# Kernel tuning notes

Hardware: AMD Instinct MI355X
Metric: run time of the kernel (lower is better)

Reference implementation:

```python
import jax, jax.numpy as jnp
import numpy as np

N = 100000      # nodes
E = 1600000     # edges (avg degree 16)
IN = 128        # in_channels
C = 32          # out_channels per head
H = 4           # heads
NEG_SLOPE = 0.2 # PyG GATConv leaky_relu slope


def setup_inputs() -> dict:
    key = jax.random.key(0)
    k = jax.random.split(key, 6)
    x = jax.random.normal(k[0], (N, IN), jnp.float32)
    edge_index = jax.random.randint(k[1], (2, E), 0, N, jnp.int32)
    # glorot-ish init for learned params
    W = jax.random.normal(k[2], (IN, H * C), jnp.float32) * (2.0 / (IN + H * C)) ** 0.5
    att_src = jax.random.normal(k[3], (H, C), jnp.float32) * (1.0 / C) ** 0.5
    att_dst = jax.random.normal(k[4], (H, C), jnp.float32) * (1.0 / C) ** 0.5
    bias = jnp.zeros((C,), jnp.float32)
    return {"x": x, "edge_index": edge_index, "W": W,
            "att_src": att_src, "att_dst": att_dst, "bias": bias}


def reference(x, edge_index, W, att_src, att_dst, bias):
    n = x.shape[0]
    h_heads, c = att_src.shape
    # add self loops (PyG GATConv default add_self_loops=True)
    loop = jnp.arange(n, dtype=edge_index.dtype)
    src = jnp.concatenate([edge_index[0], loop])
    dst = jnp.concatenate([edge_index[1], loop])
    # shared linear projection for src and dst (single-tensor input in PyG)
    h = (x @ W).reshape(n, h_heads, c)                 # [N,H,C]
    a_src = jnp.sum(h * att_src, axis=-1)              # [N,H]
    a_dst = jnp.sum(h * att_dst, axis=-1)              # [N,H]
    # per-edge attention logits
    e = jax.nn.leaky_relu(a_src[src] + a_dst[dst], NEG_SLOPE)  # [E',H]
    # segment softmax over incoming edges of each dst node
    m = jax.ops.segment_max(e, dst, num_segments=n)    # [N,H]
    m = jax.lax.stop_gradient(jnp.where(jnp.isfinite(m), m, 0.0))
    p = jnp.exp(e - m[dst])
    denom = jax.ops.segment_sum(p, dst, num_segments=n)
    alpha = p / (denom[dst] + 1e-16)                   # [E',H]
    # weighted message scatter-add
    msg = h[src] * alpha[:, :, None]                   # [E',H,C]
    out = jax.ops.segment_sum(msg, dst, num_segments=n)  # [N,H,C]
    out = out.mean(axis=1) + bias                      # concat=False -> head mean
    return jax.nn.relu(out)                            # trailing act layer
```

## Files before the change

kernel.cpp:

```cpp
#include <hip/hip_runtime.h>

#define NODES 100000
#define NEDGE 1600000
#define ET (NEDGE + NODES)
#define INC 128
#define CC 32
#define HH 4
#define NEG 0.2f
#define NB 98

typedef __attribute__((ext_vector_type(8))) short short8;
typedef __attribute__((ext_vector_type(4))) float f32x4;
typedef __attribute__((ext_vector_type(8))) unsigned short u16x8;

static __device__ inline unsigned short f2bf(float f) {
    unsigned u = __float_as_uint(f);
    u += 0x7FFFu + ((u >> 16) & 1u);
    return (unsigned short)(u >> 16);
}
static __device__ inline float bf2f(unsigned short s) {
    return __uint_as_float((unsigned)s << 16);
}
static __device__ inline float lexp(float v) {
    v = v > 0.f ? v : NEG * v;
    return __expf(v);
}

__global__ __launch_bounds__(256) void k_proj(const float* __restrict__ x,
        const float* __restrict__ W, const float* __restrict__ att_src,
        const float* __restrict__ att_dst, unsigned short* __restrict__ hb,
        float* __restrict__ av) {
    __shared__ unsigned short Wt[128][136];
    __shared__ unsigned short Axt[8][128];
    const int tid = threadIdx.x;

    for (int i = tid; i < 128 * 128; i += 256) {
        int k = i >> 7, c = i & 127;
        Wt[c][k] = f2bf(W[i]);
    }
    for (int t = tid; t < 512; t += 256) {
        int k = t >> 2, hd = t & 3;
        float ss = 0.f, sd = 0.f;
        const float* wr = W + k * 128 + hd * 32;
        for (int c = 0; c < 32; ++c) {
            ss = fmaf(wr[c], att_src[hd * 32 + c], ss);
            sd = fmaf(wr[c], att_dst[hd * 32 + c], sd);
        }
        Axt[hd][k] = f2bf(ss);
        Axt[4 + hd][k] = f2bf(sd);
    }
    __syncthreads();

    const int w    = tid >> 6;
    const int lane = tid & 63;
    const int quad = lane >> 4;
    const int l15  = lane & 15;

    for (int base = blockIdx.x * 64; base < NODES; base += gridDim.x * 64) {
        const int arow = base + w * 16 + l15;
        short8 af[4];
        if (arow < NODES) {
            const float* xp = x + (size_t)arow * INC + quad * 8;
            #pragma unroll
            for (int kt = 0; kt < 4; ++kt) {
                float4 u = *(const float4*)(xp + kt * 32);
                float4 v = *(const float4*)(xp + kt * 32 + 4);
                short8 a;
                a[0] = (short)f2bf(u.x); a[1] = (short)f2bf(u.y);
                a[2] = (short)f2bf(u.z); a[3] = (short)f2bf(u.w);
                a[4] = (short)f2bf(v.x); a[5] = (short)f2bf(v.y);
                a[6] = (short)f2bf(v.z); a[7] = (short)f2bf(v.w);
                af[kt] = a;
            }
        } else {
            #pragma unroll
            for (int kt = 0; kt < 4; ++kt) af[kt] = (short8){0,0,0,0,0,0,0,0};
        }

        f32x4 accs[8];
        #pragma unroll
        for (int ct = 0; ct < 8; ++ct) {
            const int gcol = ct * 16 + l15;
            f32x4 acc = {0.f, 0.f, 0.f, 0.f};
            #pragma unroll
            for (int kt = 0; kt < 4; ++kt) {
                short8 bf = *(short8*)(&Wt[gcol][kt * 32 + quad * 8]);
                acc = __builtin_amdgcn_mfma_f32_16x16x32_bf16(af[kt], bf, acc, 0, 0, 0);
            }
            accs[ct] = acc;
        }

        f32x4 acc9 = {0.f, 0.f, 0.f, 0.f};
        #pragma unroll
        for (int kt = 0; kt < 4; ++kt) {
            short8 bf = (short8){0,0,0,0,0,0,0,0};
            if (l15 < 8)
                bf = *(short8*)(&Axt[l15][kt * 32 + quad * 8]);
            acc9 = __builtin_amdgcn_mfma_f32_16x16x32_bf16(af[kt], bf, acc9, 0, 0, 0);
        }

        const int orow = base + w * 16 + quad * 4;

        #pragma unroll
        for (int reg = 0; reg < 4; ++reg) {
            int r = orow + reg;
            if (r < NODES) {
                if (l15 < 8) av[(size_t)r * 8 + l15] = acc9[reg];
                ushort4 lo, hi;
                lo.x = f2bf(accs[0][reg]); lo.y = f2bf(accs[2][reg]);
                lo.z = f2bf(accs[4][reg]); lo.w = f2bf(accs[6][reg]);
                hi.x = f2bf(accs[1][reg]); hi.y = f2bf(accs[3][reg]);
                hi.z = f2bf(accs[5][reg]); hi.w = f2bf(accs[7][reg]);
                *(ushort4*)(hb + (size_t)r * INC + l15 * 4) = lo;
                *(ushort4*)(hb + (size_t)r * INC + (16 + l15) * 4) = hi;
            }
        }
    }
}

__global__ void k_rank(const int* __restrict__ ei, int* __restrict__ deg,
                       int* __restrict__ rank) {
    int e = blockIdx.x * blockDim.x + threadIdx.x;
    if (e >= ET) return;
    int d = (e < NEDGE) ? ei[NEDGE + e] : e - NEDGE;
    rank[e] = atomicAdd(&deg[d], 1);
}

__global__ __launch_bounds__(256) void k_scan_part(const int* __restrict__ deg,
                                                   int* __restrict__ partial) {
    __shared__ int red[4];
    const int t = threadIdx.x;
    const int idx0 = blockIdx.x * 1024 + t * 4;
    int s = 0;
    if (idx0 + 3 < NODES) {
        int4 v = *(const int4*)(deg + idx0);
        s = v.x + v.y + v.z + v.w;
    } else {
        for (int k = 0; k < 4; ++k) if (idx0 + k < NODES) s += deg[idx0 + k];
    }
    #pragma unroll
    for (int o = 32; o; o >>= 1) s += __shfl_down(s, o, 64);
    if ((t & 63) == 0) red[t >> 6] = s;
    __syncthreads();
    if (t == 0) partial[blockIdx.x] = red[0] + red[1] + red[2] + red[3];
}

__global__ __launch_bounds__(128) void k_scan_base(const int* __restrict__ partial,
                                                   int* __restrict__ basep) {
    __shared__ int buf[128];
    const int t = threadIdx.x;
    int v = (t < NB) ? partial[t] : 0;
    buf[t] = v;
    __syncthreads();
    for (int d = 1; d < 128; d <<= 1) {
        int u = (t >= d) ? buf[t - d] : 0;
        __syncthreads();
        buf[t] += u;
        __syncthreads();
    }
    if (t < NB) basep[t] = buf[t] - v;
}

__global__ __launch_bounds__(256) void k_scan_off(const int* __restrict__ deg,
        const int* __restrict__ basep, int* __restrict__ off) {
    __shared__ int tsum[256];
    const int t = threadIdx.x;
    const int idx0 = blockIdx.x * 1024 + t * 4;
    int v[4] = {0, 0, 0, 0};
    if (idx0 + 3 < NODES) {
        int4 q = *(const int4*)(deg + idx0);
        v[0] = q.x; v[1] = q.y; v[2] = q.z; v[3] = q.w;
    } else {
        for (int k = 0; k < 4; ++k) if (idx0 + k < NODES) v[k] = deg[idx0 + k];
    }
    const int s = v[0] + v[1] + v[2] + v[3];
    tsum[t] = s;
    __syncthreads();
    for (int d = 1; d < 256; d <<= 1) {
        int u = (t >= d) ? tsum[t - d] : 0;
        __syncthreads();
        tsum[t] += u;
        __syncthreads();
    }
    int pre = basep[blockIdx.x] + tsum[t] - s;
    int4 o;
    o.x = pre;
    o.y = o.x + v[0];
    o.z = o.y + v[1];
    o.w = o.z + v[2];
    if (idx0 + 3 < NODES) {
        *(int4*)(off + idx0) = o;
    } else {
        const int oa[4] = {o.x, o.y, o.z, o.w};
        for (int k = 0; k < 4; ++k) if (idx0 + k < NODES) off[idx0 + k] = oa[k];
    }
}

__global__ void k_place(const int* __restrict__ ei, const int* __restrict__ rank,
        const int* __restrict__ off, int* __restrict__ csr4) {
    int e = blockIdx.x * blockDim.x + threadIdx.x;
    if (e >= ET) return;
    int s, d;
    if (e < NEDGE) { s = ei[e]; d = ei[NEDGE + e]; } else { s = d = e - NEDGE; }
    csr4[off[d] + rank[e]] = s;
}

__global__ __launch_bounds__(256) void k_scatter(const int* __restrict__ csr4,
        const int* __restrict__ off, const int* __restrict__ deg,
        const unsigned short* __restrict__ hb, const float* __restrict__ av,
        const float* __restrict__ bias, float* __restrict__ out) {
    const int n = blockIdx.x * 16 + (threadIdx.x >> 4);
    const int l = threadIdx.x & 15;
    const int cbase = off[n];
    const int cnt = deg[n];
    const float4 ad = *(const float4*)(av + (size_t)n * 8 + 4);

    float acc[8] = {0.f,0.f,0.f,0.f,0.f,0.f,0.f,0.f};
    float den[4] = {0.f,0.f,0.f,0.f};

    int i = 0;
    for (; i + 2 <= cnt; i += 2) {
        int s0 = csr4[cbase + i];
        int s1 = csr4[cbase + i + 1];
        float4 as0 = *(const float4*)(av + (size_t)s0 * 8);
        float4 as1 = *(const float4*)(av + (size_t)s1 * 8);
        u16x8 h0 = *(const u16x8*)(hb + (size_t)s0 * INC + l * 8);
        u16x8 h1 = *(const u16x8*)(hb + (size_t)s1 * INC + l * 8);
        float p0 = lexp(as0.x + ad.x), p1 = lexp(as0.y + ad.y);
        float p2 = lexp(as0.z + ad.z), p3 = lexp(as0.w + ad.w);
        den[0] += p0; den[1] += p1; den[2] += p2; den[3] += p3;
        acc[0] = fmaf(p0, bf2f(h0[0]), acc[0]);
        acc[1] = fmaf(p1, bf2f(h0[1]), acc[1]);
        acc[2] = fmaf(p2, bf2f(h0[2]), acc[2]);
        acc[3] = fmaf(p3, bf2f(h0[3]), acc[3]);
        acc[4] = fmaf(p0, bf2f(h0[4]), acc[4]);
        acc[5] = fmaf(p1, bf2f(h0[5]), acc[5]);
        acc[6] = fmaf(p2, bf2f(h0[6]), acc[6]);
        acc[7] = fmaf(p3, bf2f(h0[7]), acc[7]);
        float q0 = lexp(as1.x + ad.x), q1 = lexp(as1.y + ad.y);
        float q2 = lexp(as1.z + ad.z), q3 = lexp(as1.w + ad.w);
        den[0] += q0; den[1] += q1; den[2] += q2; den[3] += q3;
        acc[0] = fmaf(q0, bf2f(h1[0]), acc[0]);
        acc[1] = fmaf(q1, bf2f(h1[1]), acc[1]);
        acc[2] = fmaf(q2, bf2f(h1[2]), acc[2]);
        acc[3] = fmaf(q3, bf2f(h1[3]), acc[3]);
        acc[4] = fmaf(q0, bf2f(h1[4]), acc[4]);
        acc[5] = fmaf(q1, bf2f(h1[5]), acc[5]);
        acc[6] = fmaf(q2, bf2f(h1[6]), acc[6]);
        acc[7] = fmaf(q3, bf2f(h1[7]), acc[7]);
    }
    if (i < cnt) {
        int s0 = csr4[cbase + i];
        float4 as0 = *(const float4*)(av + (size_t)s0 * 8);
        u16x8 h0 = *(const u16x8*)(hb + (size_t)s0 * INC + l * 8);
        float p0 = lexp(as0.x + ad.x), p1 = lexp(as0.y + ad.y);
        float p2 = lexp(as0.z + ad.z), p3 = lexp(as0.w + ad.w);
        den[0] += p0; den[1] += p1; den[2] += p2; den[3] += p3;
        acc[0] = fmaf(p0, bf2f(h0[0]), acc[0]);
        acc[1] = fmaf(p1, bf2f(h0[1]), acc[1]);
        acc[2] = fmaf(p2, bf2f(h0[2]), acc[2]);
        acc[3] = fmaf(p3, bf2f(h0[3]), acc[3]);
        acc[4] = fmaf(p0, bf2f(h0[4]), acc[4]);
        acc[5] = fmaf(p1, bf2f(h0[5]), acc[5]);
        acc[6] = fmaf(p2, bf2f(h0[6]), acc[6]);
        acc[7] = fmaf(p3, bf2f(h0[7]), acc[7]);
    }

    float r0 = 1.f / (den[0] + 1e-16f);
    float r1 = 1.f / (den[1] + 1e-16f);
    float r2 = 1.f / (den[2] + 1e-16f);
    float r3 = 1.f / (den[3] + 1e-16f);
    float o0 = 0.25f * (acc[0]*r0 + acc[1]*r1 + acc[2]*r2 + acc[3]*r3)
             + bias[2*l];
    float o1 = 0.25f * (acc[4]*r0 + acc[5]*r1 + acc[6]*r2 + acc[7]*r3)
             + bias[2*l + 1];
    float2 ov;
    ov.x = o0 > 0.f ? o0 : 0.f;
    ov.y = o1 > 0.f ? o1 : 0.f;
    *(float2*)(out + (size_t)n * CC + 2*l) = ov;
}

extern "C" void kernel_launch(void* const* d_in, const int* in_sizes, int n_in,
                              void* d_out, int out_size, void* d_ws, size_t ws_size,
                              hipStream_t stream) {
    const float* x       = (const float*)d_in[0];
    const int*   ei      = (const int*)d_in[1];
    const float* W       = (const float*)d_in[2];
    const float* att_src = (const float*)d_in[3];
    const float* att_dst = (const float*)d_in[4];
    const float* bias    = (const float*)d_in[5];
    float* out = (float*)d_out;

    int* csr4           = (int*)d_ws;
    unsigned short* hb  = (unsigned short*)(csr4 + (size_t)ET);
    float* av           = (float*)(hb + (size_t)NODES * INC);
    int* deg            = (int*)(av + (size_t)NODES * 8);
    int* off            = deg + NODES;
    int* rank           = off + NODES;
    int* partial        = rank + ET;
    int* basep          = partial + NB;

    hipMemsetAsync(deg, 0, sizeof(int) * (size_t)NODES, stream);

    k_proj<<<521, 256, 0, stream>>>(x, W, att_src, att_dst, hb, av);

    k_rank<<<(ET + 255) / 256, 256, 0, stream>>>(ei, deg, rank);
    k_scan_part<<<NB, 256, 0, stream>>>(deg, partial);
    k_scan_base<<<1, 128, 0, stream>>>(partial, basep);
    k_scan_off<<<NB, 256, 0, stream>>>(deg, basep, off);
    k_place<<<(ET + 255) / 256, 256, 0, stream>>>(ei, rank, off, csr4);

    k_scatter<<<NODES / 16, 256, 0, stream>>>(csr4, off, deg, hb, av, bias, out);
}
```

Measured before the change: 304.3 us.

## Fuse degree counting into projection, use atomic cursor placement, batch CSR loads

Degree counting moves into the projection kernel through a grid-stride atomic loop, so the separate rank kernel and the per-edge rank array go away. CSR placement now takes slots with atomicAdd on a per-node cursor seeded from the offsets, instead of reading the stored ranks. The gather kernel loads 16 neighbour indices cooperatively per group, shares them with shuffles, and prefetches the next batch. The cost is atomic contention during placement and a nondeterministic neighbour order, which changes float summation order.

New measurement: 453.2 us. 1.49x slower.

```diff
diff --git a/kernel.cpp b/kernel.cpp
--- a/kernel.cpp
+++ b/kernel.cpp
@@ -28,11 +28,17 @@
 
 __global__ __launch_bounds__(256) void k_proj(const float* __restrict__ x,
         const float* __restrict__ W, const float* __restrict__ att_src,
-        const float* __restrict__ att_dst, unsigned short* __restrict__ hb,
-        float* __restrict__ av) {
+        const float* __restrict__ att_dst, const int* __restrict__ ei,
+        unsigned short* __restrict__ hb, float* __restrict__ av,
+        int* __restrict__ deg) {
     __shared__ unsigned short Wt[128][136];
     __shared__ unsigned short Axt[8][128];
     const int tid = threadIdx.x;
+
+    for (int e = blockIdx.x * blockDim.x + tid; e < ET; e += gridDim.x * blockDim.x) {
+        int d = (e < NEDGE) ? ei[NEDGE + e] : e - NEDGE;
+        atomicAdd(&deg[d], 1);
+    }
 
     for (int i = tid; i < 128 * 128; i += 256) {
         int k = i >> 7, c = i & 127;
@@ -118,14 +124,6 @@
     }
 }
 
-__global__ void k_rank(const int* __restrict__ ei, int* __restrict__ deg,
-                       int* __restrict__ rank) {
-    int e = blockIdx.x * blockDim.x + threadIdx.x;
-    if (e >= ET) return;
-    int d = (e < NEDGE) ? ei[NEDGE + e] : e - NEDGE;
-    rank[e] = atomicAdd(&deg[d], 1);
-}
-
 __global__ __launch_bounds__(256) void k_scan_part(const int* __restrict__ deg,
                                                    int* __restrict__ partial) {
     __shared__ int red[4];
@@ -162,7 +160,8 @@
 }
 
 __global__ __launch_bounds__(256) void k_scan_off(const int* __restrict__ deg,
-        const int* __restrict__ basep, int* __restrict__ off) {
+        const int* __restrict__ basep, int* __restrict__ off,
+        int* __restrict__ cursor) {
     __shared__ int tsum[256];
     const int t = threadIdx.x;
     const int idx0 = blockIdx.x * 1024 + t * 4;
@@ -190,19 +189,24 @@
     o.w = o.z + v[2];
     if (idx0 + 3 < NODES) {
         *(int4*)(off + idx0) = o;
+        *(int4*)(cursor + idx0) = o;
     } else {
         const int oa[4] = {o.x, o.y, o.z, o.w};
-        for (int k = 0; k < 4; ++k) if (idx0 + k < NODES) off[idx0 + k] = oa[k];
-    }
-}
-
-__global__ void k_place(const int* __restrict__ ei, const int* __restrict__ rank,
-        const int* __restrict__ off, int* __restrict__ csr4) {
+        for (int k = 0; k < 4; ++k) if (idx0 + k < NODES) {
+            off[idx0 + k] = oa[k];
+            cursor[idx0 + k] = oa[k];
+        }
+    }
+}
+
+__global__ void k_place(const int* __restrict__ ei, int* __restrict__ cursor,
+                        int* __restrict__ csr4) {
     int e = blockIdx.x * blockDim.x + threadIdx.x;
     if (e >= ET) return;
     int s, d;
     if (e < NEDGE) { s = ei[e]; d = ei[NEDGE + e]; } else { s = d = e - NEDGE; }
-    csr4[off[d] + rank[e]] = s;
+    int slot = atomicAdd(&cursor[d], 1);
+    csr4[slot] = s;
 }
 
 __global__ __launch_bounds__(256) void k_scatter(const int* __restrict__ csr4,
@@ -218,53 +222,38 @@
     float acc[8] = {0.f,0.f,0.f,0.f,0.f,0.f,0.f,0.f};
     float den[4] = {0.f,0.f,0.f,0.f};
 
-    int i = 0;
-    for (; i + 2 <= cnt; i += 2) {
-        int s0 = csr4[cbase + i];
-        int s1 = csr4[cbase + i + 1];
-        float4 as0 = *(const float4*)(av + (size_t)s0 * 8);
-        float4 as1 = *(const float4*)(av + (size_t)s1 * 8);
-        u16x8 h0 = *(const u16x8*)(hb + (size_t)s0 * INC + l * 8);
-        u16x8 h1 = *(const u16x8*)(hb + (size_t)s1 * INC + l * 8);
-        float p0 = lexp(as0.x + ad.x), p1 = lexp(as0.y + ad.y);
-        float p2 = lexp(as0.z + ad.z), p3 = lexp(as0.w + ad.w);
-        den[0] += p0; den[1] += p1; den[2] += p2; den[3] += p3;
-        acc[0] = fmaf(p0, bf2f(h0[0]), acc[0]);
-        acc[1] = fmaf(p1, bf2f(h0[1]), acc[1]);
-        acc[2] = fmaf(p2, bf2f(h0[2]), acc[2]);
-        acc[3] = fmaf(p3, bf2f(h0[3]), acc[3]);
-        acc[4] = fmaf(p0, bf2f(h0[4]), acc[4]);
-        acc[5] = fmaf(p1, bf2f(h0[5]), acc[5]);
-        acc[6] = fmaf(p2, bf2f(h0[6]), acc[6]);
-        acc[7] = fmaf(p3, bf2f(h0[7]), acc[7]);
-        float q0 = lexp(as1.x + ad.x), q1 = lexp(as1.y + ad.y);
-        float q2 = lexp(as1.z + ad.z), q3 = lexp(as1.w + ad.w);
-        den[0] += q0; den[1] += q1; den[2] += q2; den[3] += q3;
-        acc[0] = fmaf(q0, bf2f(h1[0]), acc[0]);
-        acc[1] = fmaf(q1, bf2f(h1[1]), acc[1]);
-        acc[2] = fmaf(q2, bf2f(h1[2]), acc[2]);
-        acc[3] = fmaf(q3, bf2f(h1[3]), acc[3]);
-        acc[4] = fmaf(q0, bf2f(h1[4]), acc[4]);
-        acc[5] = fmaf(q1, bf2f(h1[5]), acc[5]);
-        acc[6] = fmaf(q2, bf2f(h1[6]), acc[6]);
-        acc[7] = fmaf(q3, bf2f(h1[7]), acc[7]);
-    }
-    if (i < cnt) {
-        int s0 = csr4[cbase + i];
-        float4 as0 = *(const float4*)(av + (size_t)s0 * 8);
-        u16x8 h0 = *(const u16x8*)(hb + (size_t)s0 * INC + l * 8);
-        float p0 = lexp(as0.x + ad.x), p1 = lexp(as0.y + ad.y);
-        float p2 = lexp(as0.z + ad.z), p3 = lexp(as0.w + ad.w);
-        den[0] += p0; den[1] += p1; den[2] += p2; den[3] += p3;
-        acc[0] = fmaf(p0, bf2f(h0[0]), acc[0]);
-        acc[1] = fmaf(p1, bf2f(h0[1]), acc[1]);
-        acc[2] = fmaf(p2, bf2f(h0[2]), acc[2]);
-        acc[3] = fmaf(p3, bf2f(h0[3]), acc[3]);
-        acc[4] = fmaf(p0, bf2f(h0[4]), acc[4]);
-        acc[5] = fmaf(p1, bf2f(h0[5]), acc[5]);
-        acc[6] = fmaf(p2, bf2f(h0[6]), acc[6]);
-        acc[7] = fmaf(p3, bf2f(h0[7]), acc[7]);
-    }
+#define EDGE(J) { \
+    int s_ = __shfl(sl, (J), 16); \
+    float4 as_ = *(const float4*)(av + (size_t)s_ * 8); \
+    u16x8 h_ = *(const u16x8*)(hb + (size_t)s_ * INC + l * 8); \
+    float p0 = lexp(as_.x + ad.x), p1 = lexp(as_.y + ad.y); \
+    float p2 = lexp(as_.z + ad.z), p3 = lexp(as_.w + ad.w); \
+    den[0] += p0; den[1] += p1; den[2] += p2; den[3] += p3; \
+    acc[0] = fmaf(p0, bf2f(h_[0]), acc[0]); \
+    acc[1] = fmaf(p1, bf2f(h_[1]), acc[1]); \
+    acc[2] = fmaf(p2, bf2f(h_[2]), acc[2]); \
+    acc[3] = fmaf(p3, bf2f(h_[3]), acc[3]); \
+    acc[4] = fmaf(p0, bf2f(h_[4]), acc[4]); \
+    acc[5] = fmaf(p1, bf2f(h_[5]), acc[5]); \
+    acc[6] = fmaf(p2, bf2f(h_[6]), acc[6]); \
+    acc[7] = fmaf(p3, bf2f(h_[7]), acc[7]); }
+
+    int sl = (l < cnt) ? csr4[cbase + l] : 0;
+
+    for (int base = 0; base < cnt; base += 16) {
+        const int nxt = base + 16;
+        int sln = 0;
+        if (nxt + l < cnt) sln = csr4[cbase + nxt + l];
+        const int rem = cnt - base;
+        if (rem >= 16) {
+            #pragma unroll 8
+            for (int j = 0; j < 16; ++j) EDGE(j)
+        } else {
+            for (int j = 0; j < rem; ++j) EDGE(j)
+        }
+        sl = sln;
+    }
+#undef EDGE
 
     float r0 = 1.f / (den[0] + 1e-16f);
     float r1 = 1.f / (den[1] + 1e-16f);
@@ -296,19 +285,18 @@
     float* av           = (float*)(hb + (size_t)NODES * INC);
     int* deg            = (int*)(av + (size_t)NODES * 8);
     int* off            = deg + NODES;
-    int* rank           = off + NODES;
-    int* partial        = rank + ET;
+    int* cursor         = off + NODES;
+    int* partial        = cursor + NODES;
     int* basep          = partial + NB;
 
     hipMemsetAsync(deg, 0, sizeof(int) * (size_t)NODES, stream);
 
-    k_proj<<<521, 256, 0, stream>>>(x, W, att_src, att_dst, hb, av);
-
-    k_rank<<<(ET + 255) / 256, 256, 0, stream>>>(ei, deg, rank);
+    k_proj<<<521, 256, 0, stream>>>(x, W, att_src, att_dst, ei, hb, av, deg);
+
     k_scan_part<<<NB, 256, 0, stream>>>(deg, partial);
     k_scan_base<<<1, 128, 0, stream>>>(partial, basep);
-    k_scan_off<<<NB, 256, 0, stream>>>(deg, basep, off);
-    k_place<<<(ET + 255) / 256, 256, 0, stream>>>(ei, rank, off, csr4);
+    k_scan_off<<<NB, 256, 0, stream>>>(deg, basep, off, cursor);
+    k_place<<<(ET + 255) / 256, 256, 0, stream>>>(ei, cursor, csr4);
 
     k_scatter<<<NODES / 16, 256, 0, stream>>>(csr4, off, deg, hb, av, bias, out);
 }
```
